# Performance work log

Hardware: AMD Instinct MI355X
Metric: run time of the kernel (lower is better)

The kernel has to match this reference:

```python
import jax, jax.numpy as jnp
import numpy as np

N, E, F, H, G, EPS = 50000, 500000, 128, 192, 256, 1e-5


def setup_inputs() -> dict:
    key = jax.random.key(0)
    ks = jax.random.split(key, 16)
    s = 0.05
    return {
        "x": jax.random.normal(ks[0], (N, F), jnp.float32),
        "edge_index": jax.random.randint(ks[1], (2, E), 0, N),
        "batch": jnp.sort(jax.random.randint(ks[2], (N,), 0, G)),
        "num_graphs": G,
        "w_rel0": jax.random.normal(ks[3], (H, F)) * s,
        "b_rel0": jnp.zeros((H,), jnp.float32),
        "w_root0": jax.random.normal(ks[4], (H, F)) * s,
        "w_rel": jax.random.normal(ks[5], (3, H, H)) * s,
        "b_rel": jnp.zeros((3, H), jnp.float32),
        "w_root": jax.random.normal(ks[6], (3, H, H)) * s,
        "bn_gamma": jnp.ones((4, H), jnp.float32),
        "bn_beta": jnp.zeros((4, H), jnp.float32),
        "head_w1": jax.random.normal(ks[7], (H, H)) * s,
        "head_b1": jnp.zeros((H,), jnp.float32),
        "head_w2": jax.random.normal(ks[8], (H, H)) * s,
        "head_b2": jnp.zeros((H,), jnp.float32),
        "out_w": jax.random.normal(ks[9], (1, H)) * s,
        "out_b": jnpp if False else jnp.zeros((1,), jnp.float32),
    }


def _conv_bn_relu(x, src, dst, n_nodes, wr, br, wroot, gamma, beta):
    # PyG GraphConv: out_i = lin_rel(sum_{j->i} x_j) + lin_root(x_i)
    agg = jax.ops.segment_sum(x[src], dst, num_segments=n_nodes)  # [N, d]
    h = agg @ wr.T + br + x @ wroot.T                             # [N, H]
    mu = h.mean(axis=0)
    var = h.var(axis=0)  # biased, as torch BN train mode
    h = (h - mu) * jax.lax.rsqrt(var + EPS) * gamma + beta
    return jax.nn.relu(h)


def reference(x, edge_index, batch, num_graphs, w_rel0, b_rel0, w_root0,
              w_rel, b_rel, w_root, bn_gamma, bn_beta,
              head_w1, head_b1, head_w2, head_b2, out_w, out_b):
    src, dst = edge_index[0], edge_index[1]
    n_nodes = x.shape[0]
    h = _conv_bn_relu(x, src, dst, n_nodes, w_rel0, b_rel0, w_root0,
                      bn_gamma[0], bn_beta[0])
    for i in range(3):
        h = _conv_bn_relu(h, src, dst, n_nodes, w_rel[i], b_rel[i], w_root[i],
                          bn_gamma[i + 1], bn_beta[i + 1])
    # global mean pool per graph
    sums = jax.ops.segment_sum(h, batch, num_segments=num_graphs)   # [G, H]
    cnts = jax.ops.segment_sum(jnp.ones((n_nodes,), h.dtype), batch,
                               num_segments=num_graphs)
    g = sums / jnp.maximum(cnts, 1.0)[:, None]
    # MLP head (dropout = eval) + output linear
    hh = jax.nn.relu(g @ head_w1.T + head_b1) @ head_w2.T + head_b2
    out = hh @ out_w.T + out_b                                      # [G, 1]
    return out[:, 0]
```

## Files before the change

kernel.cpp:

```cpp
#include <hip/hip_runtime.h>

#define HD 192
#define FD0 128
#define NG 256
#define BNEPS 1e-5f

#define STAT_S  1048576.0f
#define STAT_IS (1.0f / 1048576.0f)
#define QS  2048.0f
#define QIS (1.0f / 2048.0f)

typedef unsigned short u16;
typedef __attribute__((ext_vector_type(8))) short bf16x8;
typedef __attribute__((ext_vector_type(4))) float f32x4;

static inline int idiv(int a, int b) { return (a + b - 1) / b; }

__device__ __forceinline__ float b2f(u16 u) {
    unsigned int v = ((unsigned int)u) << 16;
    return __builtin_bit_cast(float, v);
}
__device__ __forceinline__ u16 f2b(float f) {
    unsigned int x = __builtin_bit_cast(unsigned int, f);
    return (u16)((x + 0x7FFFu + ((x >> 16) & 1u)) >> 16);
}
__device__ __forceinline__ short f2q(float v) {
    return (short)__float2int_rn(fmaxf(fminf(v, 15.9f), -15.9f) * QS);
}

__device__ __forceinline__ void async_cp16(const void* g, void* l) {
    __builtin_amdgcn_global_load_lds(
        (const __attribute__((address_space(1))) unsigned int*)g,
        (__attribute__((address_space(3))) unsigned int*)l, 16, 0, 0);
}

__global__ __launch_bounds__(256) void convert_x(const float* __restrict__ in,
    u16* __restrict__ xb, short* __restrict__ xq, int n4)
{
    const int i = blockIdx.x * 256 + threadIdx.x;
    if (i >= n4) return;
    const float4 v = ((const float4*)in)[i];
    u16 o[4] = { f2b(v.x), f2b(v.y), f2b(v.z), f2b(v.w) };
    ((ushort4*)xb)[i] = *(ushort4*)o;
    short q[4] = { f2q(v.x), f2q(v.y), f2q(v.z), f2q(v.w) };
    ((short4*)xq)[i] = *(short4*)q;
}

__global__ __launch_bounds__(256) void pack_weights(const float* __restrict__ wr,
    const float* __restrict__ wt, u16* __restrict__ out, int K)
{
    const int idx = blockIdx.x * 256 + threadIdx.x;
    const int total = HD * 2 * K;
    if (idx >= total) return;
    const int NCk = K / 16;
    const int j  = idx & 7;
    const int t  = idx >> 3;
    const int c  = t & 15;
    const int kg = (t >> 4) & 3;
    const int rest  = t >> 6;
    const int f6    = rest % 6;
    const int rest2 = rest / 6;
    const int chunk   = rest2 % NCk;
    const int colhalf = rest2 / NCk;
    const int col = colhalf * 96 + f6 * 16 + c;
    const int k   = chunk * 32 + kg * 8 + j;
    const float v = (k < K) ? wr[(size_t)col * K + k] : wt[(size_t)col * K + (k - K)];
    out[idx] = f2b(v);
}

__global__ __launch_bounds__(256) void transpose_w(const float* __restrict__ w,
                                                   float* __restrict__ wt)
{
    const int idx = blockIdx.x * 256 + threadIdx.x;
    if (idx >= HD * HD) return;
    const int t = idx % HD, k = idx / HD;
    wt[idx] = w[(size_t)t * HD + k];
}

__global__ __launch_bounds__(256) void hist_kernel(const int* __restrict__ dst,
                                                   int* __restrict__ deg, int E)
{
    const int e = blockIdx.x * 256 + threadIdx.x;
    if (e < E) atomicAdd(&deg[dst[e]], 1);
}

__global__ __launch_bounds__(256) void scan_partial(const int* __restrict__ deg,
                                                    int* __restrict__ psum, int N)
{
    __shared__ int s[256];
    const int t = threadIdx.x;
    const int i = blockIdx.x * 256 + t;
    s[t] = (i < N) ? deg[i] : 0;
    __syncthreads();
    for (int off = 128; off > 0; off >>= 1) {
        if (t < off) s[t] += s[t + off];
        __syncthreads();
    }
    if (t == 0) psum[blockIdx.x] = s[0];
}

__global__ __launch_bounds__(256) void scan_small(int* __restrict__ psum, int M)
{
    __shared__ int s[256];
    const int t = threadIdx.x;
    s[t] = (t < M) ? psum[t] : 0;
    __syncthreads();
    for (int off = 1; off < 256; off <<= 1) {
        const int u = (t >= off) ? s[t - off] : 0;
        __syncthreads();
        s[t] += u;
        __syncthreads();
    }
    if (t < M) psum[t] = (t == 0) ? 0 : s[t - 1];
}

__global__ __launch_bounds__(256) void scan_expand(const int* __restrict__ deg,
    const int* __restrict__ psum, int* __restrict__ rowptr, int N, int E)
{
    __shared__ int s[256];
    const int t = threadIdx.x;
    const int i = blockIdx.x * 256 + t;
    const int v = (i < N) ? deg[i] : 0;
    s[t] = v;
    __syncthreads();
    for (int off = 1; off < 256; off <<= 1) {
        const int u = (t >= off) ? s[t - off] : 0;
        __syncthreads();
        s[t] += u;
        __syncthreads();
    }
    if (i < N) rowptr[i] = psum[blockIdx.x] + s[t] - v;
    if (i == N - 1) rowptr[N] = E;
}

__global__ __launch_bounds__(256) void fill_kernel(const int* __restrict__ src,
    const int* __restrict__ dst, const int* __restrict__ rowptr,
    int* __restrict__ cursor, int* __restrict__ eidx, int E)
{
    const int e = blockIdx.x * 256 + threadIdx.x;
    if (e >= E) return;
    const int d = dst[e];
    const int p = atomicAdd(&cursor[d], 1);
    eidx[rowptr[d] + p] = src[e];
}

template<int FD>
__global__ __launch_bounds__(256) void gather_kernel(
    const short* __restrict__ hq, const int* __restrict__ rowptr,
    const int* __restrict__ eidx, u16* __restrict__ aggb, int N)
{
    constexpr int GW = FD / 32;
    constexpr int ND = GW / 2;
    const int lane = threadIdx.x & 63;
    const int half = lane >> 5;
    const int g    = lane & 31;
    const int n    = blockIdx.x * 4 + (threadIdx.x >> 6);
    if (n >= N) return;
    const int beg = rowptr[n], end = rowptr[n + 1];

    int acc[GW];
#pragma unroll
    for (int i = 0; i < GW; ++i) acc[i] = 0;

    int j = beg + half;
    for (; j + 2 < end; j += 4) {
        const int s0 = eidx[j], s1 = eidx[j + 2];
        const unsigned int* p0 = (const unsigned int*)(hq + (size_t)s0 * FD + g * GW);
        const unsigned int* p1 = (const unsigned int*)(hq + (size_t)s1 * FD + g * GW);
        unsigned int u0[ND], u1[ND];
#pragma unroll
        for (int d = 0; d < ND; ++d) { u0[d] = p0[d]; u1[d] = p1[d]; }
#pragma unroll
        for (int d = 0; d < ND; ++d) {
            acc[2*d]   += (int)(short)(u0[d] & 0xffffu) + (int)(short)(u1[d] & 0xffffu);
            acc[2*d+1] += (((int)u0[d]) >> 16) + (((int)u1[d]) >> 16);
        }
    }
    if (j < end) {
        const int s0 = eidx[j];
        const unsigned int* p0 = (const unsigned int*)(hq + (size_t)s0 * FD + g * GW);
#pragma unroll
        for (int d = 0; d < ND; ++d) {
            const unsigned int u = p0[d];
            acc[2*d]   += (int)(short)(u & 0xffffu);
            acc[2*d+1] += ((int)u) >> 16;
        }
    }
#pragma unroll
    for (int i = 0; i < GW; ++i) acc[i] += __shfl_xor(acc[i], 32);

    if (half == 0) {
        unsigned int* q = (unsigned int*)(aggb + (size_t)n * FD + g * GW);
#pragma unroll
        for (int d = 0; d < ND; ++d) {
            const u16 lo = f2b((float)acc[2*d]   * QIS);
            const u16 hi = f2b((float)acc[2*d+1] * QIS);
            q[d] = (unsigned int)lo | ((unsigned int)hi << 16);
        }
    }
}

template<int K1, int K2>
__global__ __launch_bounds__(256, 2) void gemm_mfma(
    const u16* __restrict__ A1, const u16* __restrict__ A2,
    const u16* __restrict__ Wb, const float* __restrict__ bias,
    u16* __restrict__ Hout, long long* __restrict__ statsq, int N)
{
    constexpr int KC  = K1 + K2;
    constexpr int NC  = KC / 32;
    constexpr int NC1 = K1 / 32;
    __shared__ u16 bsh[96 * KC];

    const int tid  = threadIdx.x;
    const int wave = tid >> 6, lane = tid & 63;
    const int c = lane & 15, kg = lane >> 4;
    const int colhalf = blockIdx.x & 1;
    const int row0 = (blockIdx.x >> 1) * 192 + wave * 48;

    {
        const u16* wsrc = Wb + (size_t)colhalf * 96 * KC + tid * 8;
        u16* ldst = bsh + tid * 8;
        constexpr int NST = (96 * KC) / (256 * 8);
#pragma unroll
        for (int i = 0; i < NST; ++i)
            async_cp16(wsrc + i * 2048, ldst + i * 2048);
    }

    int arc[3];
#pragma unroll
    for (int m = 0; m < 3; ++m) {
        const int r = row0 + m * 16 + c;
        arc[m] = r < N ? r : N - 1;
    }

    f32x4 acc[3][6];
#pragma unroll
    for (int m = 0; m < 3; ++m)
#pragma unroll
        for (int f = 0; f < 6; ++f) acc[m][f] = (f32x4){0.f, 0.f, 0.f, 0.f};

    __syncthreads();

#pragma unroll 2
    for (int ch = 0; ch < NC; ++ch) {
        const int kk = ch * 32;
        bf16x8 a[3];
#pragma unroll
        for (int m = 0; m < 3; ++m) {
            const u16* p = (ch < NC1) ? (A1 + (size_t)arc[m] * K1 + kk + kg * 8)
                                      : (A2 + (size_t)arc[m] * K2 + (kk - K1) + kg * 8);
            a[m] = *(const bf16x8*)p;
        }
#pragma unroll
        for (int f = 0; f < 6; ++f) {
            const bf16x8 b = *(const bf16x8*)&bsh[ch * 3072 + f * 512 + kg * 128 + c * 8];
#pragma unroll
            for (int m = 0; m < 3; ++m)
                acc[m][f] = __builtin_amdgcn_mfma_f32_16x16x32_bf16(a[m], b, acc[m][f], 0, 0, 0);
        }
    }

    float s1v[6], s2v[6];
#pragma unroll
    for (int f = 0; f < 6; ++f) { s1v[f] = 0.f; s2v[f] = 0.f; }

#pragma unroll
    for (int f = 0; f < 6; ++f) {
        const int col = colhalf * 96 + f * 16 + c;
        const float bv = bias[col];
#pragma unroll
        for (int m = 0; m < 3; ++m)
#pragma unroll
            for (int r = 0; r < 4; ++r) {
                const int orow = row0 + m * 16 + kg * 4 + r;
                if (orow < N) {
                    const float v = acc[m][f][r] + bv;
                    s1v[f] += v;
                    s2v[f] += v * v;
                    Hout[(size_t)orow * HD + col] = f2b(v);
                }
            }
    }
#pragma unroll
    for (int f = 0; f < 6; ++f) {
        s1v[f] += __shfl_xor(s1v[f], 16); s1v[f] += __shfl_xor(s1v[f], 32);
        s2v[f] += __shfl_xor(s2v[f], 16); s2v[f] += __shfl_xor(s2v[f], 32);
    }
    __syncthreads();
    float* red = (float*)bsh;
    if (kg == 0) {
#pragma unroll
        for (int f = 0; f < 6; ++f) {
            red[wave * 96 + f * 16 + c]       = s1v[f];
            red[384 + wave * 96 + f * 16 + c] = s2v[f];
        }
    }
    __syncthreads();
    if (tid < 96) {
        float a1 = 0.f, a2 = 0.f;
#pragma unroll
        for (int w = 0; w < 4; ++w) { a1 += red[w * 96 + tid]; a2 += red[384 + w * 96 + tid]; }
        const int col = colhalf * 96 + tid;
        atomicAdd((unsigned long long*)&statsq[col],
                  (unsigned long long)(long long)llrintf(a1 * STAT_S));
        atomicAdd((unsigned long long*)&statsq[HD + col],
                  (unsigned long long)(long long)llrintf(a2 * STAT_S));
    }
}

__global__ __launch_bounds__(256) void norm_relu(const u16* __restrict__ hpre,
    u16* __restrict__ hb, short* __restrict__ hq,
    const long long* __restrict__ statsq,
    const float* __restrict__ gamma, const float* __restrict__ beta, int N)
{
    __shared__ float sc[HD], sh[HD];
    const int t = threadIdx.x;
    if (t < HD) {
        const float inv = 1.0f / (float)N;
        const float sum = (float)statsq[t] * STAT_IS;
        const float sq  = (float)statsq[HD + t] * STAT_IS;
        const float mu  = sum * inv;
        const float var = sq * inv - mu * mu;
        const float s   = gamma[t] * rsqrtf(var + BNEPS);
        sc[t] = s; sh[t] = beta[t] - mu * s;
    }
    __syncthreads();
    const int idx = blockIdx.x * 256 + t;
    const int total = N * (HD / 8);
    if (idx >= total) return;
    const int c8 = idx % (HD / 8);
    uint4 packed = ((const uint4*)hpre)[idx];
    const u16* pu = (const u16*)&packed;
    u16 ob[8]; short oq[8];
#pragma unroll
    for (int j = 0; j < 8; ++j) {
        const int cc = c8 * 8 + j;
        const float v = fmaxf(0.f, fmaf(b2f(pu[j]), sc[cc], sh[cc]));
        ob[j] = f2b(v);
        oq[j] = (short)__float2int_rn(fminf(v, 15.9f) * QS);
    }
    ((uint4*)hb)[idx] = *(uint4*)ob;
    ((uint4*)hq)[idx] = *(uint4*)oq;
}

__global__ __launch_bounds__(256) void pool_head_kernel(
    const u16* __restrict__ h, const int* __restrict__ batch, int N,
    const float* __restrict__ w1t, const float* __restrict__ b1,
    const float* __restrict__ w2t, const float* __restrict__ b2,
    const float* __restrict__ ow, const float* __restrict__ ob,
    float* __restrict__ out)
{
    __shared__ float pp[8][HD];
    __shared__ float gv[HD];
    __shared__ float h1[HD];
    __shared__ float h2[HD];
    const int g = blockIdx.x;
    const int t = threadIdx.x;
    const int rp = t >> 5;
    const int o  = t & 31;

    int lo = 0, hi = N;
    while (lo < hi) { int m = (lo + hi) >> 1; if (batch[m] < g) lo = m + 1; else hi = m; }
    const int start = lo;
    hi = N;
    while (lo < hi) { int m = (lo + hi) >> 1; if (batch[m] < g + 1) lo = m + 1; else hi = m; }
    const int end = lo;

    float facc[8];
#pragma unroll
    for (int i = 0; i < 8; ++i) facc[i] = 0.f;
    if (o < 24) {
        for (int r = start + rp; r < end; r += 8) {
            const uint4 pv = *(const uint4*)(h + (size_t)r * HD + o * 8);
            const u16* pu = (const u16*)&pv;
#pragma unroll
            for (int i = 0; i < 8; ++i) facc[i] += b2f(pu[i]);
        }
#pragma unroll
        for (int i = 0; i < 8; ++i) pp[rp][o * 8 + i] = facc[i];
    }
    __syncthreads();
    if (t < HD) {
        float s = 0.f;
#pragma unroll
        for (int r = 0; r < 8; ++r) s += pp[r][t];
        gv[t] = s / fmaxf((float)(end - start), 1.0f);
    }
    __syncthreads();
    if (t < HD) {
        float acc = b1[t];
#pragma unroll 4
        for (int k = 0; k < HD; ++k)
            acc = fmaf(gv[k], w1t[k * HD + t], acc);
        h1[t] = fmaxf(acc, 0.f);
    }
    __syncthreads();
    if (t < HD) {
        float acc = b2[t];
#pragma unroll 4
        for (int k = 0; k < HD; ++k)
            acc = fmaf(h1[k], w2t[k * HD + t], acc);
        h2[t] = acc * ow[t];
    }
    __syncthreads();
    if (t < 64) {
        float s = h2[t] + h2[t + 64] + h2[t + 128];
#pragma unroll
        for (int d = 1; d < 64; d <<= 1) s += __shfl_xor(s, d);
        if (t == 0) out[g] = s + ob[0];
    }
}

extern "C" void kernel_launch(void* const* d_in, const int* in_sizes, int n_in,
                              void* d_out, int out_size, void* d_ws, size_t ws_size,
                              hipStream_t stream)
{
    const float* x       = (const float*)d_in[0];
    const int*   ei      = (const int*)d_in[1];
    const int*   batch   = (const int*)d_in[2];
    const float* w_rel0  = (const float*)d_in[4];
    const float* b_rel0  = (const float*)d_in[5];
    const float* w_root0 = (const float*)d_in[6];
    const float* w_rel   = (const float*)d_in[7];
    const float* b_rel   = (const float*)d_in[8];
    const float* w_root  = (const float*)d_in[9];
    const float* bn_g    = (const float*)d_in[10];
    const float* bn_b    = (const float*)d_in[11];
    const float* hw1     = (const float*)d_in[12];
    const float* hb1     = (const float*)d_in[13];
    const float* hw2     = (const float*)d_in[14];
    const float* hb2     = (const float*)d_in[15];
    const float* ow      = (const float*)d_in[16];
    const float* ob      = (const float*)d_in[17];
    float* out = (float*)d_out;

    const int N = in_sizes[0] / FD0;
    const int E = in_sizes[1] / 2;
    const int* src = ei;
    const int* dst = ei + E;
    const int M = idiv(N, 256);

    char* ws = (char*)d_ws;
    size_t off = 0;
    u16*   xb   = (u16*)(ws + off);   off += (size_t)N * FD0 * 2;
    short* xq   = (short*)(ws + off); off += (size_t)N * FD0 * 2;
    u16*   hb   = (u16*)(ws + off);   off += (size_t)N * HD * 2;
    short* hq   = (short*)(ws + off); off += (size_t)N * HD * 2;
    u16*   aggb = (u16*)(ws + off);   off += (size_t)N * HD * 2;
    u16*   hpre = (u16*)(ws + off);   off += (size_t)N * HD * 2;
    u16*   wp0  = (u16*)(ws + off);   off += (size_t)HD * 2 * FD0 * 2;
    u16*   wp123= (u16*)(ws + off);   off += (size_t)3 * HD * 2 * HD * 2;
    off = (off + 15) & ~(size_t)15;
    float* w1t = (float*)(ws + off); off += (size_t)HD * HD * 4;
    float* w2t = (float*)(ws + off); off += (size_t)HD * HD * 4;
    long long* statsq = (long long*)(ws + off); off += 2 * HD * sizeof(long long);
    int*   rowptr = (int*)(ws + off); off += (size_t)(N + 1) * 4;
    int*   deg    = (int*)(ws + off); off += (size_t)N * 4;
    int*   psum   = (int*)(ws + off); off += (size_t)M * 4;
    int*   eidx   = (int*)(ws + off); off += (size_t)E * 4;

    const dim3 b256(256);

    convert_x<<<idiv(N * FD0 / 4, 256), b256, 0, stream>>>(x, xb, xq, N * FD0 / 4);
    pack_weights<<<idiv(HD * 2 * FD0, 256), b256, 0, stream>>>(w_rel0, w_root0, wp0, FD0);
    for (int i = 0; i < 3; ++i)
        pack_weights<<<idiv(HD * 2 * HD, 256), b256, 0, stream>>>(
            w_rel + (size_t)i * HD * HD, w_root + (size_t)i * HD * HD,
            wp123 + (size_t)i * HD * 2 * HD, HD);
    transpose_w<<<idiv(HD * HD, 256), b256, 0, stream>>>(hw1, w1t);
    transpose_w<<<idiv(HD * HD, 256), b256, 0, stream>>>(hw2, w2t);
    hipMemsetAsync(deg, 0, (size_t)N * sizeof(int), stream);
    hist_kernel<<<idiv(E, 256), b256, 0, stream>>>(dst, deg, E);
    scan_partial<<<M, b256, 0, stream>>>(deg, psum, N);
    scan_small<<<1, b256, 0, stream>>>(psum, M);
    scan_expand<<<M, b256, 0, stream>>>(deg, psum, rowptr, N, E);
    hipMemsetAsync(deg, 0, (size_t)N * sizeof(int), stream);
    fill_kernel<<<idiv(E, 256), b256, 0, stream>>>(src, dst, rowptr, deg, eidx, E);

    hipMemsetAsync(statsq, 0, 2 * HD * sizeof(long long), stream);
    gather_kernel<FD0><<<idiv(N, 4), b256, 0, stream>>>(xq, rowptr, eidx, aggb, N);
    gemm_mfma<FD0, FD0><<<idiv(N, 192) * 2, b256, 0, stream>>>(aggb, xb, wp0, b_rel0,
                                                               hpre, statsq, N);
    norm_relu<<<idiv(N * (HD / 8), 256), b256, 0, stream>>>(hpre, hb, hq, statsq,
                                                            bn_g, bn_b, N);

    for (int i = 0; i < 3; ++i) {
        hipMemsetAsync(statsq, 0, 2 * HD * sizeof(long long), stream);
        gather_kernel<HD><<<idiv(N, 4), b256, 0, stream>>>(hq, rowptr, eidx, aggb, N);
        gemm_mfma<HD, HD><<<idiv(N, 192) * 2, b256, 0, stream>>>(
            aggb, hb, wp123 + (size_t)i * HD * 2 * HD,
            b_rel + (size_t)i * HD, hpre, statsq, N);
        norm_relu<<<idiv(N * (HD / 8), 256), b256, 0, stream>>>(hpre, hb, hq, statsq,
            bn_g + (size_t)(i + 1) * HD, bn_b + (size_t)(i + 1) * HD, N);
    }

    pool_head_kernel<<<NG, b256, 0, stream>>>(hb, batch, N, w1t, hb1, w2t, hb2,
                                              ow, ob, out);
}
```

Measured before the change: 455.2 us.

## Widen GEMM tile to full 192 columns and unroll gather by four edges

The MFMA GEMM now runs 512-thread blocks that each compute all 192 output columns for 256 rows, with the whole packed weight matrix staged in LDS. The weight packing is reordered to match. The aim is to read each A row once instead of once per column half. The gather kernel now processes four neighbour edges per iteration instead of two, which raises memory-level parallelism. The trade-offs are larger LDS use (up to 144KB for the 384-K layers) and more accumulator registers per wave, which lowers occupancy to one block per CU.

```diff
diff --git a/kernel.cpp b/kernel.cpp
--- a/kernel.cpp
+++ b/kernel.cpp
@@ -52,17 +52,14 @@
     const int idx = blockIdx.x * 256 + threadIdx.x;
     const int total = HD * 2 * K;
     if (idx >= total) return;
-    const int NCk = K / 16;
     const int j  = idx & 7;
     const int t  = idx >> 3;
     const int c  = t & 15;
     const int kg = (t >> 4) & 3;
-    const int rest  = t >> 6;
-    const int f6    = rest % 6;
-    const int rest2 = rest / 6;
-    const int chunk   = rest2 % NCk;
-    const int colhalf = rest2 / NCk;
-    const int col = colhalf * 96 + f6 * 16 + c;
+    const int rest = t >> 6;
+    const int fglob = rest % 12;
+    const int chunk = rest / 12;
+    const int col = fglob * 16 + c;
     const int k   = chunk * 32 + kg * 8 + j;
     const float v = (k < K) ? wr[(size_t)col * K + k] : wt[(size_t)col * K + (k - K)];
     out[idx] = f2b(v);
@@ -163,20 +160,25 @@
     for (int i = 0; i < GW; ++i) acc[i] = 0;
 
     int j = beg + half;
-    for (; j + 2 < end; j += 4) {
-        const int s0 = eidx[j], s1 = eidx[j + 2];
+    for (; j + 6 < end; j += 8) {
+        const int s0 = eidx[j],     s1 = eidx[j + 2];
+        const int s2 = eidx[j + 4], s3 = eidx[j + 6];
         const unsigned int* p0 = (const unsigned int*)(hq + (size_t)s0 * FD + g * GW);
         const unsigned int* p1 = (const unsigned int*)(hq + (size_t)s1 * FD + g * GW);
-        unsigned int u0[ND], u1[ND];
-#pragma unroll
-        for (int d = 0; d < ND; ++d) { u0[d] = p0[d]; u1[d] = p1[d]; }
+        const unsigned int* p2 = (const unsigned int*)(hq + (size_t)s2 * FD + g * GW);
+        const unsigned int* p3 = (const unsigned int*)(hq + (size_t)s3 * FD + g * GW);
+        unsigned int u0[ND], u1[ND], u2[ND], u3[ND];
+#pragma unroll
+        for (int d = 0; d < ND; ++d) { u0[d] = p0[d]; u1[d] = p1[d]; u2[d] = p2[d]; u3[d] = p3[d]; }
 #pragma unroll
         for (int d = 0; d < ND; ++d) {
-            acc[2*d]   += (int)(short)(u0[d] & 0xffffu) + (int)(short)(u1[d] & 0xffffu);
-            acc[2*d+1] += (((int)u0[d]) >> 16) + (((int)u1[d]) >> 16);
-        }
-    }
-    if (j < end) {
+            acc[2*d]   += (int)(short)(u0[d] & 0xffffu) + (int)(short)(u1[d] & 0xffffu)
+                        + (int)(short)(u2[d] & 0xffffu) + (int)(short)(u3[d] & 0xffffu);
+            acc[2*d+1] += (((int)u0[d]) >> 16) + (((int)u1[d]) >> 16)
+                        + (((int)u2[d]) >> 16) + (((int)u3[d]) >> 16);
+        }
+    }
+    for (; j < end; j += 2) {
         const int s0 = eidx[j];
         const unsigned int* p0 = (const unsigned int*)(hq + (size_t)s0 * FD + g * GW);
 #pragma unroll
@@ -201,7 +203,7 @@
 }
 
 template<int K1, int K2>
-__global__ __launch_bounds__(256, 2) void gemm_mfma(
+__global__ __launch_bounds__(512, 1) void gemm_mfma(
     const u16* __restrict__ A1, const u16* __restrict__ A2,
     const u16* __restrict__ Wb, const float* __restrict__ bias,
     u16* __restrict__ Hout, long long* __restrict__ statsq, int N)
@@ -209,67 +211,64 @@
     constexpr int KC  = K1 + K2;
     constexpr int NC  = KC / 32;
     constexpr int NC1 = K1 / 32;
-    __shared__ u16 bsh[96 * KC];
+    __shared__ u16 bsh[HD * KC];
 
     const int tid  = threadIdx.x;
     const int wave = tid >> 6, lane = tid & 63;
     const int c = lane & 15, kg = lane >> 4;
-    const int colhalf = blockIdx.x & 1;
-    const int row0 = (blockIdx.x >> 1) * 192 + wave * 48;
+    const int row0 = blockIdx.x * 256 + wave * 32;
 
     {
-        const u16* wsrc = Wb + (size_t)colhalf * 96 * KC + tid * 8;
+        constexpr int NST = (HD * KC) / (512 * 8);
+        const u16* wsrc = Wb + tid * 8;
         u16* ldst = bsh + tid * 8;
-        constexpr int NST = (96 * KC) / (256 * 8);
 #pragma unroll
         for (int i = 0; i < NST; ++i)
-            async_cp16(wsrc + i * 2048, ldst + i * 2048);
-    }
-
-    int arc[3];
-#pragma unroll
-    for (int m = 0; m < 3; ++m) {
+            async_cp16(wsrc + i * 4096, ldst + i * 4096);
+    }
+
+    int arc[2];
+#pragma unroll
+    for (int m = 0; m < 2; ++m) {
         const int r = row0 + m * 16 + c;
         arc[m] = r < N ? r : N - 1;
     }
 
-    f32x4 acc[3][6];
-#pragma unroll
-    for (int m = 0; m < 3; ++m)
-#pragma unroll
-        for (int f = 0; f < 6; ++f) acc[m][f] = (f32x4){0.f, 0.f, 0.f, 0.f};
-
-    __syncthreads();
-
-#pragma unroll 2
+    f32x4 acc[2][12];
+#pragma unroll
+    for (int m = 0; m < 2; ++m)
+#pragma unroll
+        for (int f = 0; f < 12; ++f) acc[m][f] = (f32x4){0.f, 0.f, 0.f, 0.f};
+
+    __syncthreads();
+
     for (int ch = 0; ch < NC; ++ch) {
         const int kk = ch * 32;
-        bf16x8 a[3];
-#pragma unroll
-        for (int m = 0; m < 3; ++m) {
+        bf16x8 a[2];
+#pragma unroll
+        for (int m = 0; m < 2; ++m) {
             const u16* p = (ch < NC1) ? (A1 + (size_t)arc[m] * K1 + kk + kg * 8)
                                       : (A2 + (size_t)arc[m] * K2 + (kk - K1) + kg * 8);
             a[m] = *(const bf16x8*)p;
         }
 #pragma unroll
-        for (int f = 0; f < 6; ++f) {
-            const bf16x8 b = *(const bf16x8*)&bsh[ch * 3072 + f * 512 + kg * 128 + c * 8];
-#pragma unroll
-            for (int m = 0; m < 3; ++m)
-                acc[m][f] = __builtin_amdgcn_mfma_f32_16x16x32_bf16(a[m], b, acc[m][f], 0, 0, 0);
-        }
-    }
-
-    float s1v[6], s2v[6];
-#pragma unroll
-    for (int f = 0; f < 6; ++f) { s1v[f] = 0.f; s2v[f] = 0.f; }
-
-#pragma unroll
-    for (int f = 0; f < 6; ++f) {
-        const int col = colhalf * 96 + f * 16 + c;
+        for (int f = 0; f < 12; ++f) {
+            const bf16x8 b = *(const bf16x8*)&bsh[ch * 6144 + f * 512 + kg * 128 + c * 8];
+            acc[0][f] = __builtin_amdgcn_mfma_f32_16x16x32_bf16(a[0], b, acc[0][f], 0, 0, 0);
+            acc[1][f] = __builtin_amdgcn_mfma_f32_16x16x32_bf16(a[1], b, acc[1][f], 0, 0, 0);
+        }
+    }
+
+    float s1v[12], s2v[12];
+#pragma unroll
+    for (int f = 0; f < 12; ++f) { s1v[f] = 0.f; s2v[f] = 0.f; }
+
+#pragma unroll
+    for (int f = 0; f < 12; ++f) {
+        const int col = f * 16 + c;
         const float bv = bias[col];
 #pragma unroll
-        for (int m = 0; m < 3; ++m)
+        for (int m = 0; m < 2; ++m)
 #pragma unroll
             for (int r = 0; r < 4; ++r) {
                 const int orow = row0 + m * 16 + kg * 4 + r;
@@ -282,7 +281,7 @@
             }
     }
 #pragma unroll
-    for (int f = 0; f < 6; ++f) {
+    for (int f = 0; f < 12; ++f) {
         s1v[f] += __shfl_xor(s1v[f], 16); s1v[f] += __shfl_xor(s1v[f], 32);
         s2v[f] += __shfl_xor(s2v[f], 16); s2v[f] += __shfl_xor(s2v[f], 32);
     }
@@ -290,20 +289,22 @@
     float* red = (float*)bsh;
     if (kg == 0) {
 #pragma unroll
-        for (int f = 0; f < 6; ++f) {
-            red[wave * 96 + f * 16 + c]       = s1v[f];
-            red[384 + wave * 96 + f * 16 + c] = s2v[f];
-        }
-    }
-    __syncthreads();
-    if (tid < 96) {
+        for (int f = 0; f < 12; ++f) {
+            red[wave * HD + f * 16 + c]            = s1v[f];
+            red[8 * HD + wave * HD + f * 16 + c]   = s2v[f];
+        }
+    }
+    __syncthreads();
+    if (tid < HD) {
         float a1 = 0.f, a2 = 0.f;
 #pragma unroll
-        for (int w = 0; w < 4; ++w) { a1 += red[w * 96 + tid]; a2 += red[384 + w * 96 + tid]; }
-        const int col = colhalf * 96 + tid;
-        atomicAdd((unsigned long long*)&statsq[col],
+        for (int w = 0; w < 8; ++w) {
+            a1 += red[w * HD + tid];
+            a2 += red[8 * HD + w * HD + tid];
+        }
+        atomicAdd((unsigned long long*)&statsq[tid],
                   (unsigned long long)(long long)llrintf(a1 * STAT_S));
-        atomicAdd((unsigned long long*)&statsq[HD + col],
+        atomicAdd((unsigned long long*)&statsq[HD + tid],
                   (unsigned long long)(long long)llrintf(a2 * STAT_S));
     }
 }
@@ -459,7 +460,7 @@
     int*   psum   = (int*)(ws + off); off += (size_t)M * 4;
     int*   eidx   = (int*)(ws + off); off += (size_t)E * 4;
 
-    const dim3 b256(256);
+    const dim3 b256(256), b512(512);
 
     convert_x<<<idiv(N * FD0 / 4, 256), b256, 0, stream>>>(x, xb, xq, N * FD0 / 4);
     pack_weights<<<idiv(HD * 2 * FD0, 256), b256, 0, stream>>>(w_rel0, w_root0, wp0, FD0);
@@ -479,15 +480,15 @@
 
     hipMemsetAsync(statsq, 0, 2 * HD * sizeof(long long), stream);
     gather_kernel<FD0><<<idiv(N, 4), b256, 0, stream>>>(xq, rowptr, eidx, aggb, N);
-    gemm_mfma<FD0, FD0><<<idiv(N, 192) * 2, b256, 0, stream>>>(aggb, xb, wp0, b_rel0,
-                                                               hpre, statsq, N);
+    gemm_mfma<FD0, FD0><<<idiv(N, 256), b512, 0, stream>>>(aggb, xb, wp0, b_rel0,
+                                                           hpre, statsq, N);
     norm_relu<<<idiv(N * (HD / 8), 256), b256, 0, stream>>>(hpre, hb, hq, statsq,
                                                             bn_g, bn_b, N);
 
     for (int i = 0; i < 3; ++i) {
         hipMemsetAsync(statsq, 0, 2 * HD * sizeof(long long), stream);
         gather_kernel<HD><<<idiv(N, 4), b256, 0, stream>>>(hq, rowptr, eidx, aggb, N);
-        gemm_mfma<HD, HD><<<idiv(N, 192) * 2, b256, 0, stream>>>(
+        gemm_mfma<HD, HD><<<idiv(N, 256), b512, 0, stream>>>(
             aggb, hb, wp123 + (size_t)i * HD * 2 * HD,
             b_rel + (size_t)i * HD, hpre, statsq, N);
         norm_relu<<<idiv(N * (HD / 8), 256), b256, 0, stream>>>(hpre, hb, hq, statsq,
```

After: 405.4 us. 10.9% less time.
